# Kernel optimization log

Measured on AMD Instinct MI355X. Metric: run time of the kernel, lower is better.

The kernel has to match this reference:

```python
import jax, jax.numpy as jnp
import numpy as np

WS = 17  # window_size


def _conv(x, w, padding, groups=1):
    return jax.lax.conv_general_dilated(
        x, w, window_strides=(1, 1), padding=padding,
        dimension_numbers=("NCHW", "OIHW", "NCHW"),
        feature_group_count=groups)


def setup_inputs() -> dict:
    key = jax.random.key(0)
    ks = jax.random.split(key, 5)
    B, C, H, W = 4, 64, 510, 510
    x = jax.random.normal(ks[0], (B, C, H, W), dtype=jnp.float32)
    # Sobel depthwise kernel, exactly as init_sobel_weights
    sobel = jnp.array([[-1.0, 0.0, 1.0], [-2.0, 0.0, 2.0], [-1.0, 0.0, 1.0]],
                      dtype=jnp.float32)
    sobel_w = jnp.tile(sobel[None, None], (C, 1, 1, 1))  # [C,1,3,3]
    w1 = jax.random.normal(ks[1], (16, C, 3, 3), jnp.float32) * 0.04
    b1 = jax.random.normal(ks[2], (16,), jnp.float32) * 0.01
    w2 = jax.random.normal(ks[3], (1, 16, 1, 1), jnp.float32) * 0.1
    b2 = jax.random.normal(ks[4], (1,), jnp.float32) * 0.01
    return {"x": x, "sobel_w": sobel_w, "w1": w1, "b1": b1, "w2": w2, "b2": b2}


def reference(x, sobel_w, w1, b1, w2, b2):
    B, C, H, W = x.shape
    pad_h = (-H) % WS
    pad_w = (-W) % WS
    x = jnp.pad(x, ((0, 0), (0, 0), (0, pad_h), (0, pad_w)))
    Hp, Wp = H + pad_h, W + pad_w
    nh, nw = Hp // WS, Wp // WS
    # F.unfold with kernel=stride=WS on NCHW == non-overlapping window split.
    # Window order is row-major over (nh, nw), matching unfold's column order.
    xw = (x.reshape(B, C, nh, WS, nw, WS)
           .transpose(0, 2, 4, 1, 3, 5)
           .reshape(B * nh * nw, C, WS, WS))
    # depthwise 3x3 sobel filter, padding=1
    freq = _conv(xw, sobel_w, [(1, 1), (1, 1)], groups=C)
    # mask generator: Conv(C->16,3x3) + ReLU + Conv(16->1,1x1) + Sigmoid
    h = jax.nn.relu(_conv(freq, w1, [(1, 1), (1, 1)]) + b1[None, :, None, None])
    mask = jax.nn.sigmoid(_conv(h, w2, [(0, 0), (0, 0)]) + b2[None, :, None, None])
    mask = jnp.clip(mask, 0.05, 0.95)
    # F.fold with non-overlapping windows; divisor fold(unfold(ones)) == 1,
    # so the divide / nan_to_num are identities.
    attn = (mask.reshape(B, nh, nw, 1, WS, WS)
                .transpose(0, 3, 1, 4, 2, 5)
                .reshape(B, 1, Hp, Wp))
    return attn[:, :, :H, :W]
```

## Files before the change

kernel.cpp:

```cpp
#include <hip/hip_runtime.h>


#define WSZ 17
#define PS  19
#define PSS (PS * PS)
#define NT  512
#define CH  (510 * 510)

typedef __attribute__((ext_vector_type(8))) _Float16 f16x8;
typedef __attribute__((ext_vector_type(2))) _Float16 f16x2;
typedef __attribute__((ext_vector_type(4))) float f32x4;
typedef __attribute__((ext_vector_type(2))) float f32x2;

__device__ __forceinline__ int swz(int off) {
    return off ^ (((off >> 7) & 7) << 4);
}

__device__ __forceinline__ unsigned short f2h(float f) {
    _Float16 h = (_Float16)f;
    unsigned short u;
    __builtin_memcpy(&u, &h, 2);
    return u;
}

__device__ __forceinline__ f16x2 pkrtz(float a, float b) {
    auto r = __builtin_amdgcn_cvt_pkrtz(a, b);
    f16x2 o;
    __builtin_memcpy(&o, &r, 4);
    return o;
}

__device__ __forceinline__ int dpp_shr1_i(int v) {
    return __builtin_amdgcn_update_dpp(0, v, 0x138, 0xf, 0xf, true);
}
__device__ __forceinline__ int dpp_shl1_i(int v) {
    return __builtin_amdgcn_update_dpp(0, v, 0x130, 0xf, 0xf, true);
}
__device__ __forceinline__ float dpp_shr1(float v) {
    return __int_as_float(dpp_shr1_i(__float_as_int(v)));
}
__device__ __forceinline__ float dpp_shl1(float v) {
    return __int_as_float(dpp_shl1_i(__float_as_int(v)));
}

#define GLD8(d0,d1,d2,d3,d4,d5,d6,d7, o0,o1,o2,o3, sp)      \
    asm volatile(                                            \
        "global_load_dword %0, %8, %12\n\t"                  \
        "global_load_dword %1, %8, %12 offset:2040\n\t"      \
        "global_load_dword %2, %9, %12\n\t"                  \
        "global_load_dword %3, %9, %12 offset:2040\n\t"      \
        "global_load_dword %4, %10, %12\n\t"                 \
        "global_load_dword %5, %10, %12 offset:2040\n\t"     \
        "global_load_dword %6, %11, %12\n\t"                 \
        "global_load_dword %7, %11, %12 offset:2040\n\t"     \
        : "+v"(d0),"+v"(d1),"+v"(d2),"+v"(d3),               \
          "+v"(d4),"+v"(d5),"+v"(d6),"+v"(d7)                \
        : "v"(o0),"v"(o1),"v"(o2),"v"(o3),"s"(sp))

#define GLD9(d0,d1,d2,d3,d4,d5,d6,d7,d8, o0,o1,o2,o3,o4, sp) \
    asm volatile(                                            \
        "global_load_dword %0, %9, %14\n\t"                  \
        "global_load_dword %1, %9, %14 offset:2040\n\t"      \
        "global_load_dword %2, %10, %14\n\t"                 \
        "global_load_dword %3, %10, %14 offset:2040\n\t"     \
        "global_load_dword %4, %11, %14\n\t"                 \
        "global_load_dword %5, %11, %14 offset:2040\n\t"     \
        "global_load_dword %6, %12, %14\n\t"                 \
        "global_load_dword %7, %12, %14 offset:2040\n\t"     \
        "global_load_dword %8, %13, %14\n\t"                 \
        : "+v"(d0),"+v"(d1),"+v"(d2),"+v"(d3),"+v"(d4),      \
          "+v"(d5),"+v"(d6),"+v"(d7),"+v"(d8)                \
        : "v"(o0),"v"(o1),"v"(o2),"v"(o3),"v"(o4),"s"(sp))

__global__ void prep_w1(const float* __restrict__ w1, unsigned short* __restrict__ wt) {
    const int dij = blockIdx.x >> 1;
    const int ks  = blockIdx.x & 1;
    const int l   = threadIdx.x;
    const int m   = l & 15;
    const int kb  = ks * 32 + 8 * (l >> 4);
    unsigned short v[8];
#pragma unroll
    for (int jj = 0; jj < 8; ++jj)
        v[jj] = f2h(w1[m * 576 + (kb + jj) * 9 + dij]);
    f16x8 o;
    __builtin_memcpy(&o, v, 16);
    ((f16x8*)wt)[blockIdx.x * 64 + l] = o;
}

__global__ __launch_bounds__(NT, 4)
void fasa_mfma(const float* __restrict__ x,
               const float* __restrict__ sobel_w,
               const unsigned short* __restrict__ wt,
               const float* __restrict__ b1,
               const float* __restrict__ w2,
               const float* __restrict__ b2,
               float* __restrict__ out)
{
    __shared__ __align__(16) char frq[PSS * 128];

    const int t    = threadIdx.x;
    const int lane = t & 63;
    const int wave = __builtin_amdgcn_readfirstlane(t >> 6);

    const int bid = blockIdx.x;
    const int win = (bid & 7) * 450 + (bid >> 3);
    const int b   = win / 900;
    const int rem = win % 900;
    const int h0  = (rem / 30) * WSZ;
    const int w0  = (rem % 30) * WSZ;

    for (int u = t; u < 72 * 8; u += NT) {
        int r = u >> 3, k = u & 7;
        int row;
        if      (r < 19) row = r;
        else if (r < 38) row = 342 + (r - 19);
        else if (r < 55) row = (r - 37) * PS;
        else             row = (r - 54) * PS + 18;
        *(f32x4*)(frq + row * 128 + k * 16) = (f32x4){0.f, 0.f, 0.f, 0.f};
    }

    const float sw0 = sobel_w[0], sw1 = sobel_w[1], sw2 = sobel_w[2];
    const float sw3 = sobel_w[3], sw4 = sobel_w[4], sw5 = sobel_w[5];
    const float sw6 = sobel_w[6], sw7 = sobel_w[7], sw8 = sobel_w[8];
    const bool fast = (sw1 == 0.f) && (sw4 == 0.f) && (sw7 == 0.f) &&
                      (sw0 == -sw2) && (sw3 == -sw5) && (sw6 == -sw8);
    const f16x2 sw2h = {(_Float16)sw2, (_Float16)sw2};
    const f16x2 sw5h = {(_Float16)sw5, (_Float16)sw5};
    const f16x2 sw8h = {(_Float16)sw8, (_Float16)sw8};

    const int j   = lane & 31;
    const int grp = lane >> 5;
    const bool jac = (j < 17);

    const float* sp00 = x + ((size_t)(b * 64 + 4 * wave)) * CH
                          + (size_t)h0 * 510 + w0;
    const float* sp01 = sp00 + (size_t)CH;
    const float* sp10 = sp00 + (size_t)32 * CH;
    const float* sp11 = sp10 + (size_t)CH;

    const unsigned v0 = (unsigned)((grp * 2 * CH + j) * 4);
    const unsigned vk0 = v0,           vk1 = v0 + 4080u,  vk2 = v0 + 8160u;
    const unsigned vk3 = v0 + 12240u,  vk4 = v0 + 16320u, vk5 = v0 + 20400u;
    const unsigned vk6 = v0 + 24480u,  vk7 = v0 + 28560u, vk8 = v0 + 32640u;

    float xA[17], yA[17], xB[17], yB[17];
#pragma unroll
    for (int i = 0; i < 17; ++i) { xA[i] = 0.f; yA[i] = 0.f; xB[i] = 0.f; yB[i] = 0.f; }

    if (jac) {
        GLD8(xA[0],xA[1],xA[2],xA[3],xA[4],xA[5],xA[6],xA[7], vk0,vk1,vk2,vk3, sp00);
        GLD9(xA[8],xA[9],xA[10],xA[11],xA[12],xA[13],xA[14],xA[15],xA[16],
             vk4,vk5,vk6,vk7,vk8, sp00);
        GLD8(yA[0],yA[1],yA[2],yA[3],yA[4],yA[5],yA[6],yA[7], vk0,vk1,vk2,vk3, sp01);
        GLD9(yA[8],yA[9],yA[10],yA[11],yA[12],yA[13],yA[14],yA[15],yA[16],
             vk4,vk5,vk6,vk7,vk8, sp01);
        GLD8(xB[0],xB[1],xB[2],xB[3],xB[4],xB[5],xB[6],xB[7], vk0,vk1,vk2,vk3, sp10);
        GLD9(xB[8],xB[9],xB[10],xB[11],xB[12],xB[13],xB[14],xB[15],xB[16],
             vk4,vk5,vk6,vk7,vk8, sp10);
        GLD8(yB[0],yB[1],yB[2],yB[3],yB[4],yB[5],yB[6],yB[7], vk0,vk1,vk2,vk3, sp11);
        GLD9(yB[8],yB[9],yB[10],yB[11],yB[12],yB[13],yB[14],yB[15],yB[16],
             vk4,vk5,vk6,vk7,vk8, sp11);
    }

    auto DOSOBEL = [&](const float* xr, const float* yr, int q) {
        const int pr = 2 * wave + grp + 16 * q;
        const int pairOff = pr * 4;
        if (fast) {
            f16x2 xh[17];
#pragma unroll
            for (int i = 0; i < 17; ++i)
                xh[i] = pkrtz(xr[i], yr[i]);
            const f16x2 zero = {(_Float16)0.f, (_Float16)0.f};
#pragma unroll
            for (int i = 0; i < 17; ++i) {
                f16x2 top = (i > 0)  ? xh[i - 1] : zero;
                f16x2 bot = (i < 16) ? xh[i + 1] : zero;
                f16x2 h = sw2h * top + sw5h * xh[i] + sw8h * bot;
                int hi;
                __builtin_memcpy(&hi, &h, 4);
                int sl = dpp_shl1_i(hi);
                int sr = dpp_shr1_i(hi);
                f16x2 hl, hr;
                __builtin_memcpy(&hl, &sl, 4);
                __builtin_memcpy(&hr, &sr, 4);
                f16x2 o = hl - hr;
                unsigned pkv;
                __builtin_memcpy(&pkv, &o, 4);
                if (jac)
                    *(unsigned*)(frq + swz(((i + 1) * PS + (j + 1)) * 128 + pairOff)) = pkv;
            }
        } else {
#pragma unroll
            for (int i = 0; i < 17; ++i) {
                f32x2 top = { (i > 0  ? xr[i - 1] : 0.f), (i > 0  ? yr[i - 1] : 0.f) };
                f32x2 mid = { xr[i],                       yr[i] };
                f32x2 bot = { (i < 16 ? xr[i + 1] : 0.f), (i < 16 ? yr[i + 1] : 0.f) };
                f32x2 p0 = sw0 * top + sw3 * mid + sw6 * bot;
                f32x2 p1 = sw1 * top + sw4 * mid + sw7 * bot;
                f32x2 p2 = sw2 * top + sw5 * mid + sw8 * bot;
                f32x2 o;
                o.x = p1.x + dpp_shr1(p0.x) + dpp_shl1(p2.x);
                o.y = p1.y + dpp_shr1(p0.y) + dpp_shl1(p2.y);
                f16x2 oh = pkrtz(o.x, o.y);
                unsigned pkv;
                __builtin_memcpy(&pkv, &oh, 4);
                if (jac)
                    *(unsigned*)(frq + swz(((i + 1) * PS + (j + 1)) * 128 + pairOff)) = pkv;
            }
        }
    };

    asm volatile("s_waitcnt vmcnt(34)" ::: "memory");
    __builtin_amdgcn_sched_barrier(0);
    DOSOBEL(xA, yA, 0);
    asm volatile("s_waitcnt vmcnt(0)" ::: "memory");
    __builtin_amdgcn_sched_barrier(0);
    DOSOBEL(xB, yB, 1);

    f16x8 wf[18];
#pragma unroll
    for (int i = 0; i < 18; ++i)
        wf[i] = ((const f16x8*)wt)[i * 64 + lane];

    float b1v[4], w2v[4];
#pragma unroll
    for (int r = 0; r < 4; ++r) {
        int m = 4 * (lane >> 4) + r;
        b1v[r] = b1[m];
        w2v[r] = w2[m];
    }
    const float b2v = b2[0];

    __syncthreads();

    const int n   = lane & 15;
    const int g16 = (lane >> 4) * 16;
    const int DOFF[9] = {0, 1, 2, PS, PS + 1, PS + 2, 2 * PS, 2 * PS + 1, 2 * PS + 2};

#pragma unroll 1
    for (int nt = wave; nt < 19; nt += 8) {
        int p  = nt * 16 + n;
        int pv = p > 288 ? 288 : p;
        int pi = pv / 17, pj = pv - pi * 17;
        int base = (pi * PS + pj) * 128 + g16;

        f32x4 acc = {0.f, 0.f, 0.f, 0.f};
#pragma unroll
        for (int d = 0; d < 9; ++d) {
            int off = base + DOFF[d] * 128;
            f16x8 bfA = *(const f16x8*)(frq + swz(off));
            f16x8 bfB = *(const f16x8*)(frq + swz(off + 64));
            acc = __builtin_amdgcn_mfma_f32_16x16x32_f16(wf[2 * d],     bfA, acc, 0, 0, 0);
            acc = __builtin_amdgcn_mfma_f32_16x16x32_f16(wf[2 * d + 1], bfB, acc, 0, 0, 0);
        }

        float part = 0.f;
#pragma unroll
        for (int r = 0; r < 4; ++r)
            part = fmaf(w2v[r], fmaxf(acc[r] + b1v[r], 0.f), part);
        part += __shfl_xor(part, 16);
        part += __shfl_xor(part, 32);

        if (lane < 16 && p < 289) {
            float pre = part + b2v;
            float s = 1.f / (1.f + expf(-pre));
            s = fminf(fmaxf(s, 0.05f), 0.95f);
            out[((size_t)(b * 510 + h0 + pi)) * 510 + (w0 + pj)] = s;
        }
    }
}

extern "C" void kernel_launch(void* const* d_in, const int* in_sizes, int n_in,
                              void* d_out, int out_size, void* d_ws, size_t ws_size,
                              hipStream_t stream) {
    const float* x       = (const float*)d_in[0];
    const float* sobel_w = (const float*)d_in[1];
    const float* w1      = (const float*)d_in[2];
    const float* b1      = (const float*)d_in[3];
    const float* w2      = (const float*)d_in[4];
    const float* b2      = (const float*)d_in[5];
    float* out = (float*)d_out;
    unsigned short* wtab = (unsigned short*)d_ws;

    prep_w1<<<dim3(18), dim3(64), 0, stream>>>(w1, wtab);
    fasa_mfma<<<dim3(3600), dim3(NT), 0, stream>>>(x, sobel_w, wtab, b1, w2, b2, out);
}
```

Baseline: 84.72 us.

## Double block threads so each wave loads one channel pair; stage weights in LDS

Raises the block size from 512 to 1024 threads so each wave loads and Sobel-filters a single channel pair instead of two. This halves the per-thread input registers. The first-layer weights now go into shared memory once per block and are read from LDS inside the MFMA loop, replacing the 18 per-lane register fragments. The aim is lower register pressure and more waves in flight to hide global load latency, at the cost of an extra 18 KB of LDS per block and more LDS reads per MFMA. With 19 tiles and 16 waves, most waves do only one MFMA tile, and the two-stage load/compute overlap inside each wave is gone.

```diff
diff --git a/kernel.cpp b/kernel.cpp
--- a/kernel.cpp
+++ b/kernel.cpp
@@ -4,7 +4,7 @@
 #define WSZ 17
 #define PS  19
 #define PSS (PS * PS)
-#define NT  512
+#define NT  1024
 #define CH  (510 * 510)
 
 typedef __attribute__((ext_vector_type(8))) _Float16 f16x8;
@@ -87,7 +87,7 @@
     ((f16x8*)wt)[blockIdx.x * 64 + l] = o;
 }
 
-__global__ __launch_bounds__(NT, 4)
+__global__ __launch_bounds__(NT, 8)
 void fasa_mfma(const float* __restrict__ x,
                const float* __restrict__ sobel_w,
                const unsigned short* __restrict__ wt,
@@ -97,6 +97,7 @@
                float* __restrict__ out)
 {
     __shared__ __align__(16) char frq[PSS * 128];
+    __shared__ __align__(16) char wlds[18432];
 
     const int t    = threadIdx.x;
     const int lane = t & 63;
@@ -109,8 +110,8 @@
     const int h0  = (rem / 30) * WSZ;
     const int w0  = (rem % 30) * WSZ;
 
-    for (int u = t; u < 72 * 8; u += NT) {
-        int r = u >> 3, k = u & 7;
+    if (t < 72 * 8) {
+        int r = t >> 3, k = t & 7;
         int row;
         if      (r < 19) row = r;
         else if (r < 38) row = 342 + (r - 19);
@@ -131,96 +132,36 @@
     const int j   = lane & 31;
     const int grp = lane >> 5;
     const bool jac = (j < 17);
-
-    const float* sp00 = x + ((size_t)(b * 64 + 4 * wave)) * CH
-                          + (size_t)h0 * 510 + w0;
-    const float* sp01 = sp00 + (size_t)CH;
-    const float* sp10 = sp00 + (size_t)32 * CH;
-    const float* sp11 = sp10 + (size_t)CH;
+    const int pr  = 2 * wave + grp;
+
+    const float* sp0 = x + ((size_t)(b * 64 + 4 * wave)) * CH
+                         + (size_t)h0 * 510 + w0;
+    const float* sp1 = sp0 + (size_t)CH;
 
     const unsigned v0 = (unsigned)((grp * 2 * CH + j) * 4);
     const unsigned vk0 = v0,           vk1 = v0 + 4080u,  vk2 = v0 + 8160u;
     const unsigned vk3 = v0 + 12240u,  vk4 = v0 + 16320u, vk5 = v0 + 20400u;
     const unsigned vk6 = v0 + 24480u,  vk7 = v0 + 28560u, vk8 = v0 + 32640u;
 
-    float xA[17], yA[17], xB[17], yB[17];
-#pragma unroll
-    for (int i = 0; i < 17; ++i) { xA[i] = 0.f; yA[i] = 0.f; xB[i] = 0.f; yB[i] = 0.f; }
+    float xA[17], yA[17];
+#pragma unroll
+    for (int i = 0; i < 17; ++i) { xA[i] = 0.f; yA[i] = 0.f; }
 
     if (jac) {
-        GLD8(xA[0],xA[1],xA[2],xA[3],xA[4],xA[5],xA[6],xA[7], vk0,vk1,vk2,vk3, sp00);
+        GLD8(xA[0],xA[1],xA[2],xA[3],xA[4],xA[5],xA[6],xA[7], vk0,vk1,vk2,vk3, sp0);
         GLD9(xA[8],xA[9],xA[10],xA[11],xA[12],xA[13],xA[14],xA[15],xA[16],
-             vk4,vk5,vk6,vk7,vk8, sp00);
-        GLD8(yA[0],yA[1],yA[2],yA[3],yA[4],yA[5],yA[6],yA[7], vk0,vk1,vk2,vk3, sp01);
+             vk4,vk5,vk6,vk7,vk8, sp0);
+        GLD8(yA[0],yA[1],yA[2],yA[3],yA[4],yA[5],yA[6],yA[7], vk0,vk1,vk2,vk3, sp1);
         GLD9(yA[8],yA[9],yA[10],yA[11],yA[12],yA[13],yA[14],yA[15],yA[16],
-             vk4,vk5,vk6,vk7,vk8, sp01);
-        GLD8(xB[0],xB[1],xB[2],xB[3],xB[4],xB[5],xB[6],xB[7], vk0,vk1,vk2,vk3, sp10);
-        GLD9(xB[8],xB[9],xB[10],xB[11],xB[12],xB[13],xB[14],xB[15],xB[16],
-             vk4,vk5,vk6,vk7,vk8, sp10);
-        GLD8(yB[0],yB[1],yB[2],yB[3],yB[4],yB[5],yB[6],yB[7], vk0,vk1,vk2,vk3, sp11);
-        GLD9(yB[8],yB[9],yB[10],yB[11],yB[12],yB[13],yB[14],yB[15],yB[16],
-             vk4,vk5,vk6,vk7,vk8, sp11);
-    }
-
-    auto DOSOBEL = [&](const float* xr, const float* yr, int q) {
-        const int pr = 2 * wave + grp + 16 * q;
-        const int pairOff = pr * 4;
-        if (fast) {
-            f16x2 xh[17];
-#pragma unroll
-            for (int i = 0; i < 17; ++i)
-                xh[i] = pkrtz(xr[i], yr[i]);
-            const f16x2 zero = {(_Float16)0.f, (_Float16)0.f};
-#pragma unroll
-            for (int i = 0; i < 17; ++i) {
-                f16x2 top = (i > 0)  ? xh[i - 1] : zero;
-                f16x2 bot = (i < 16) ? xh[i + 1] : zero;
-                f16x2 h = sw2h * top + sw5h * xh[i] + sw8h * bot;
-                int hi;
-                __builtin_memcpy(&hi, &h, 4);
-                int sl = dpp_shl1_i(hi);
-                int sr = dpp_shr1_i(hi);
-                f16x2 hl, hr;
-                __builtin_memcpy(&hl, &sl, 4);
-                __builtin_memcpy(&hr, &sr, 4);
-                f16x2 o = hl - hr;
-                unsigned pkv;
-                __builtin_memcpy(&pkv, &o, 4);
-                if (jac)
-                    *(unsigned*)(frq + swz(((i + 1) * PS + (j + 1)) * 128 + pairOff)) = pkv;
-            }
-        } else {
-#pragma unroll
-            for (int i = 0; i < 17; ++i) {
-                f32x2 top = { (i > 0  ? xr[i - 1] : 0.f), (i > 0  ? yr[i - 1] : 0.f) };
-                f32x2 mid = { xr[i],                       yr[i] };
-                f32x2 bot = { (i < 16 ? xr[i + 1] : 0.f), (i < 16 ? yr[i + 1] : 0.f) };
-                f32x2 p0 = sw0 * top + sw3 * mid + sw6 * bot;
-                f32x2 p1 = sw1 * top + sw4 * mid + sw7 * bot;
-                f32x2 p2 = sw2 * top + sw5 * mid + sw8 * bot;
-                f32x2 o;
-                o.x = p1.x + dpp_shr1(p0.x) + dpp_shl1(p2.x);
-                o.y = p1.y + dpp_shr1(p0.y) + dpp_shl1(p2.y);
-                f16x2 oh = pkrtz(o.x, o.y);
-                unsigned pkv;
-                __builtin_memcpy(&pkv, &oh, 4);
-                if (jac)
-                    *(unsigned*)(frq + swz(((i + 1) * PS + (j + 1)) * 128 + pairOff)) = pkv;
-            }
-        }
-    };
-
-    asm volatile("s_waitcnt vmcnt(34)" ::: "memory");
-    __builtin_amdgcn_sched_barrier(0);
-    DOSOBEL(xA, yA, 0);
-    asm volatile("s_waitcnt vmcnt(0)" ::: "memory");
-    __builtin_amdgcn_sched_barrier(0);
-    DOSOBEL(xB, yB, 1);
-
-    f16x8 wf[18];
-#pragma unroll
-    for (int i = 0; i < 18; ++i)
-        wf[i] = ((const f16x8*)wt)[i * 64 + lane];
+             vk4,vk5,vk6,vk7,vk8, sp1);
+    }
+
+    {
+        const f32x4* wsrc = (const f32x4*)wt;
+        f32x4* wdst = (f32x4*)wlds;
+        wdst[t] = wsrc[t];
+        if (t < 128) wdst[1024 + t] = wsrc[1024 + t];
+    }
 
     float b1v[4], w2v[4];
 #pragma unroll
@@ -231,14 +172,63 @@
     }
     const float b2v = b2[0];
 
+    asm volatile("s_waitcnt vmcnt(0)" ::: "memory");
+    __builtin_amdgcn_sched_barrier(0);
+
+    const int pairOff = pr * 4;
+    if (fast) {
+        f16x2 xh[17];
+#pragma unroll
+        for (int i = 0; i < 17; ++i)
+            xh[i] = pkrtz(xA[i], yA[i]);
+        const f16x2 zero = {(_Float16)0.f, (_Float16)0.f};
+#pragma unroll
+        for (int i = 0; i < 17; ++i) {
+            f16x2 top = (i > 0)  ? xh[i - 1] : zero;
+            f16x2 bot = (i < 16) ? xh[i + 1] : zero;
+            f16x2 h = sw2h * top + sw5h * xh[i] + sw8h * bot;
+            int hi;
+            __builtin_memcpy(&hi, &h, 4);
+            int sl = dpp_shl1_i(hi);
+            int sr = dpp_shr1_i(hi);
+            f16x2 hl, hr;
+            __builtin_memcpy(&hl, &sl, 4);
+            __builtin_memcpy(&hr, &sr, 4);
+            f16x2 o = hl - hr;
+            unsigned pkv;
+            __builtin_memcpy(&pkv, &o, 4);
+            if (jac)
+                *(unsigned*)(frq + swz(((i + 1) * PS + (j + 1)) * 128 + pairOff)) = pkv;
+        }
+    } else {
+#pragma unroll
+        for (int i = 0; i < 17; ++i) {
+            f32x2 top = { (i > 0  ? xA[i - 1] : 0.f), (i > 0  ? yA[i - 1] : 0.f) };
+            f32x2 mid = { xA[i],                       yA[i] };
+            f32x2 bot = { (i < 16 ? xA[i + 1] : 0.f), (i < 16 ? yA[i + 1] : 0.f) };
+            f32x2 p0 = sw0 * top + sw3 * mid + sw6 * bot;
+            f32x2 p1 = sw1 * top + sw4 * mid + sw7 * bot;
+            f32x2 p2 = sw2 * top + sw5 * mid + sw8 * bot;
+            f32x2 o;
+            o.x = p1.x + dpp_shr1(p0.x) + dpp_shl1(p2.x);
+            o.y = p1.y + dpp_shr1(p0.y) + dpp_shl1(p2.y);
+            f16x2 oh = pkrtz(o.x, o.y);
+            unsigned pkv;
+            __builtin_memcpy(&pkv, &oh, 4);
+            if (jac)
+                *(unsigned*)(frq + swz(((i + 1) * PS + (j + 1)) * 128 + pairOff)) = pkv;
+        }
+    }
+
     __syncthreads();
 
     const int n   = lane & 15;
     const int g16 = (lane >> 4) * 16;
     const int DOFF[9] = {0, 1, 2, PS, PS + 1, PS + 2, 2 * PS, 2 * PS + 1, 2 * PS + 2};
+    const char* wbase = wlds + lane * 16;
 
 #pragma unroll 1
-    for (int nt = wave; nt < 19; nt += 8) {
+    for (int nt = wave; nt < 19; nt += 16) {
         int p  = nt * 16 + n;
         int pv = p > 288 ? 288 : p;
         int pi = pv / 17, pj = pv - pi * 17;
@@ -250,8 +240,10 @@
             int off = base + DOFF[d] * 128;
             f16x8 bfA = *(const f16x8*)(frq + swz(off));
             f16x8 bfB = *(const f16x8*)(frq + swz(off + 64));
-            acc = __builtin_amdgcn_mfma_f32_16x16x32_f16(wf[2 * d],     bfA, acc, 0, 0, 0);
-            acc = __builtin_amdgcn_mfma_f32_16x16x32_f16(wf[2 * d + 1], bfB, acc, 0, 0, 0);
+            f16x8 wfA = *(const f16x8*)(wbase + (2 * d) * 1024);
+            f16x8 wfB = *(const f16x8*)(wbase + (2 * d + 1) * 1024);
+            acc = __builtin_amdgcn_mfma_f32_16x16x32_f16(wfA, bfA, acc, 0, 0, 0);
+            acc = __builtin_amdgcn_mfma_f32_16x16x32_f16(wfB, bfB, acc, 0, 0, 0);
         }
 
         float part = 0.f;
```

After: 303.5 us. 258% more time.
